# Kernel tuning notes

Measured on AMD Instinct MI355X. Metric: run time of the kernel, lower is better.

Reference implementation:

```python
import jax, jax.numpy as jnp
import numpy as np

N, M, D, H = 16, 1024, 64, 4  # batch, num_node, dim_in==dim_hid, num_head
NEG_SLOPE = 0.2


def setup_inputs() -> dict:
    key = jax.random.key(0)
    ks = jax.random.split(key, 10)
    s = 1.0 / np.sqrt(D)
    inp = {
        "x": jax.random.normal(ks[0], (N, M, D), dtype=jnp.float32),
        "edge": jnp.zeros((N, M, M), dtype=jnp.float32),  # unused by the module
        # stacked per-head Linear(dim_in, dim_hid) params: weight (H, D_out, D_in), bias (H, D_out)
        "Wk": (jax.random.normal(ks[1], (H, D, D), dtype=jnp.float32) * s),
        "bk": (jax.random.normal(ks[2], (H, D), dtype=jnp.float32) * s),
        "Wq": (jax.random.normal(ks[3], (H, D, D), dtype=jnp.float32) * s),
        "bq": (jax.random.normal(ks[4], (H, D), dtype=jnp.float32) * s),
        "Wv": (jax.random.normal(ks[5], (H, D, D), dtype=jnp.float32) * s),
        "bv": (jax.random.normal(ks[6], (H, D), dtype=jnp.float32) * s),
        # decoder: Linear(dim_hid*num_head -> dim_in)
        "Wdec": (jax.random.normal(ks[7], (D, H * D), dtype=jnp.float32) / np.sqrt(H * D)),
        "bdec": (jax.random.normal(ks[8], (D,), dtype=jnp.float32) / np.sqrt(H * D)),
    }
    return inp


def reference(x, edge, Wk, bk, Wq, bq, Wv, bv, Wdec, bdec):
    # x: (N, M, D). Per head h: K = x @ Wk[h].T + bk[h], etc.
    K = jnp.einsum("nmd,hed->nhme", x, Wk) + bk[None, :, None, :]  # (N,H,M,D)
    Q = jnp.einsum("nmd,hed->nhme", x, Wq) + bq[None, :, None, :]
    V = jnp.einsum("nmd,hed->nhme", x, Wv) + bv[None, :, None, :]
    # alpha[n,h,i,j] = K[n,h,i] . Q[n,h,j]  (sender=K row i, receiver=Q row j)
    alpha = jnp.einsum("nhie,nhje->nhij", K, Q)  # (N,H,M,M)
    alpha = jax.nn.leaky_relu(alpha, NEG_SLOPE)
    alpha = jax.nn.softmax(alpha, axis=-1)
    agg = jnp.einsum("nhij,nhje->nhie", alpha, V)  # (N,H,M,D)
    dx = jax.nn.leaky_relu(agg, NEG_SLOPE) - x[:, None, :, :]  # (N,H,M,D)
    # concat heads along feature dim (head 0 first): (N, M, H*D)
    dx = dx.transpose(0, 2, 1, 3).reshape(N, M, H * D)
    return dx @ Wdec.T + bdec  # (N, M, D)
```

## Files before the change

### kernel.cpp

```cpp
#include <hip/hip_runtime.h>
#include <hip/hip_bf16.h>


#define NB 16
#define MM 1024
#define DD 64
#define HH 4
#define NEG 0.2f
#define AST 72
#define DST 264

typedef __attribute__((ext_vector_type(8))) short bf16x8;
typedef __attribute__((ext_vector_type(8))) _Float16 f16x8;
typedef __attribute__((ext_vector_type(16))) float f32x16;

__device__ inline unsigned short f2bf(float f) {
  unsigned int u = __builtin_bit_cast(unsigned int, f);
  unsigned int r = (u + 0x7FFFu + ((u >> 16) & 1u)) >> 16;
  return (unsigned short)r;
}
__device__ inline unsigned short f2h(float f) {
  _Float16 h = (_Float16)f;
  return __builtin_bit_cast(unsigned short, h);
}

__global__ __launch_bounds__(256) void prep_kernel(
    const float* __restrict__ Wk, const float* __restrict__ Wq,
    const float* __restrict__ Wv, const float* __restrict__ Wdec,
    unsigned short* __restrict__ Wf) {
  const int idx = (blockIdx.x * 256 + threadIdx.x) * 4;
  const int seg = idx >> 14, local = idx & 16383;
  const float* src = seg == 0 ? Wk : seg == 1 ? Wq : seg == 2 ? Wv : Wdec;
  float4 v = *(const float4*)&src[local];
  unsigned short p[4] = {f2h(v.x), f2h(v.y), f2h(v.z), f2h(v.w)};
  *(uint2*)&Wf[idx] = *(uint2*)p;
}

__global__ __launch_bounds__(256) void proj_kernel(
    const float* __restrict__ x, const unsigned short* __restrict__ Wf,
    const float* __restrict__ bk, const float* __restrict__ bq, const float* __restrict__ bv,
    unsigned short* __restrict__ Kf, unsigned short* __restrict__ Qf,
    unsigned short* __restrict__ Vtg) {
  __shared__ unsigned short xs[64 * AST];
  __shared__ unsigned short ob[64 * AST];
  const int t = threadIdx.x;
  const int r0 = blockIdx.x * 64;
  const int combo = blockIdx.y, mat = combo >> 2, h = combo & 3;
  const int n = r0 >> 10, ml = r0 & 1023;
  const float* bias = mat == 0 ? bk : (mat == 1 ? bq : bv);

#pragma unroll
  for (int rep = 0; rep < 2; ++rep) {
    int idx = rep * 256 + t, row = idx >> 3, c8 = (idx & 7) * 8;
    float4 a = *(const float4*)&x[(size_t)(r0 + row) * DD + c8];
    float4 b = *(const float4*)&x[(size_t)(r0 + row) * DD + c8 + 4];
    unsigned short p[8] = {f2h(a.x), f2h(a.y), f2h(a.z), f2h(a.w),
                           f2h(b.x), f2h(b.y), f2h(b.z), f2h(b.w)};
    *(uint4*)&xs[row * AST + c8] = *(uint4*)p;
  }
  __syncthreads();

  const int w = t >> 6, lane = t & 63, m31 = lane & 31, hf = lane >> 5;
  const int mi = w >> 1, ne = w & 1;
  const int ecol = h * 64 + ne * 32 + m31;
  const float bb = bias[ecol];

  f32x16 C;
#pragma unroll
  for (int r = 0; r < 16; ++r) C[r] = 0.f;
#pragma unroll
  for (int ks = 0; ks < 4; ++ks) {
    f16x8 xa = *(f16x8*)&xs[(mi * 32 + m31) * AST + ks * 16 + hf * 8];
    f16x8 wb = *(const f16x8*)&Wf[(size_t)mat * 16384 + (size_t)ecol * DD + ks * 16 + hf * 8];
    C = __builtin_amdgcn_mfma_f32_32x32x16_f16(xa, wb, C, 0, 0, 0);
  }

  if (mat < 2) {
#pragma unroll
    for (int r = 0; r < 16; ++r) {
      int rr = (r & 3) + 8 * (r >> 2) + 4 * hf;
      ob[(mi * 32 + rr) * AST + ne * 32 + m31] = f2h(C[r] + bb);
    }
  } else {
#pragma unroll
    for (int r = 0; r < 16; ++r) {
      int rr = (r & 3) + 8 * (r >> 2) + 4 * hf;
      ob[(ne * 32 + m31) * AST + mi * 32 + rr] = f2bf(C[r] + bb);
    }
  }
  __syncthreads();

  if (mat < 2) {
    unsigned short* dst = mat == 0 ? Kf : Qf;
    const size_t obase = (((size_t)n * HH + h) * MM + ml) * DD;
#pragma unroll
    for (int rep = 0; rep < 2; ++rep) {
      int idx = rep * 256 + t, row = idx >> 3, c8 = (idx & 7) * 8;
      *(uint4*)&dst[obase + (size_t)row * DD + c8] = *(uint4*)&ob[row * AST + c8];
    }
  } else {
    const size_t obase = (((size_t)n * HH + h) * DD) * MM + ml;
#pragma unroll
    for (int rep = 0; rep < 2; ++rep) {
      int idx = rep * 256 + t, row = idx >> 3, c8 = (idx & 7) * 8;
      *(uint4*)&Vtg[obase + (size_t)row * MM + c8] = *(uint4*)&ob[row * AST + c8];
    }
  }
}

__global__ __launch_bounds__(256, 4) void attn_kernel(
    const unsigned short* __restrict__ Kf, const unsigned short* __restrict__ Qf,
    const unsigned short* __restrict__ Vtg, const float* __restrict__ x,
    unsigned short* __restrict__ DX) {
  __shared__ unsigned short qh[64 * AST];
  __shared__ unsigned short vt[64 * AST];
  __shared__ unsigned short ps[64 * AST];
  __shared__ float ls[64];

  const int t = threadIdx.x;
  const int w = t >> 6, lane = t & 63;
  const int m31 = lane & 31, hf = lane >> 5;
  const int ti = w >> 1, tw = w & 1;
  const int i0 = blockIdx.x * 64, h = blockIdx.y, n = blockIdx.z;
  const size_t base = (((size_t)n * HH + h) * MM) * DD;
  const size_t baseT = (((size_t)n * HH + h) * DD) * MM;

  f16x8 kfrag[4];
#pragma unroll
  for (int ks = 0; ks < 4; ++ks)
    kfrag[ks] = *(const f16x8*)&Kf[base + (size_t)(i0 + ti * 32 + m31) * DD + ks * 16 + hf * 8];

  f32x16 agg, accl;
#pragma unroll
  for (int r = 0; r < 16; ++r) { agg[r] = 0.f; accl[r] = 0.f; }
  bf16x8 ones;
#pragma unroll
  for (int r = 0; r < 8; ++r) ones[r] = (short)0x3F80;

  for (int jt = 0; jt < 16; ++jt) {
    const int j0 = jt * 64;
    __syncthreads();
#pragma unroll
    for (int rep = 0; rep < 2; ++rep) {
      int idx = rep * 256 + t, row = idx >> 3, c8 = (idx & 7) * 8;
      *(uint4*)&qh[row * AST + c8] = *(const uint4*)&Qf[base + (size_t)(j0 + row) * DD + c8];
      *(uint4*)&vt[row * AST + c8] = *(const uint4*)&Vtg[baseT + (size_t)row * MM + j0 + c8];
    }
    __syncthreads();

    f32x16 C;
#pragma unroll
    for (int r = 0; r < 16; ++r) C[r] = 0.f;
#pragma unroll
    for (int ks = 0; ks < 4; ++ks) {
      f16x8 qf = *(f16x8*)&qh[(tw * 32 + m31) * AST + ks * 16 + hf * 8];
      C = __builtin_amdgcn_mfma_f32_32x32x16_f16(kfrag[ks], qf, C, 0, 0, 0);
    }
#pragma unroll
    for (int r = 0; r < 16; ++r) {
      float s = C[r];
      s = s > 0.f ? s : NEG * s;
      int rr = (r & 3) + 8 * (r >> 2) + 4 * hf;
      ps[(ti * 32 + rr) * AST + tw * 32 + m31] = f2bf(__expf(s));
    }
    __syncthreads();

#pragma unroll
    for (int ks = 0; ks < 4; ++ks) {
      bf16x8 aP = *(bf16x8*)&ps[(ti * 32 + m31) * AST + ks * 16 + hf * 8];
      bf16x8 bV = *(bf16x8*)&vt[(tw * 32 + m31) * AST + ks * 16 + hf * 8];
      agg = __builtin_amdgcn_mfma_f32_32x32x16_bf16(aP, bV, agg, 0, 0, 0);
      if (tw == 0)
        accl = __builtin_amdgcn_mfma_f32_32x32x16_bf16(aP, ones, accl, 0, 0, 0);
    }
  }

  if (tw == 0 && m31 == 0) {
#pragma unroll
    for (int r = 0; r < 16; ++r) {
      int rr = (r & 3) + 8 * (r >> 2) + 4 * hf;
      ls[ti * 32 + rr] = accl[r];
    }
  }
  __syncthreads();

#pragma unroll
  for (int r = 0; r < 16; ++r) {
    int rr = (r & 3) + 8 * (r >> 2) + 4 * hf;
    float l = ls[ti * 32 + rr];
    float v = agg[r] / l;
    v = v > 0.f ? v : NEG * v;
    v -= x[((size_t)n * MM + i0 + ti * 32 + rr) * DD + tw * 32 + m31];
    ps[(ti * 32 + rr) * AST + tw * 32 + m31] = f2h(v);
  }
  __syncthreads();
#pragma unroll
  for (int rep = 0; rep < 2; ++rep) {
    int idx = rep * 256 + t, row = idx >> 3, c8 = (idx & 7) * 8;
    *(uint4*)&DX[((size_t)n * MM + i0 + row) * (HH * DD) + h * DD + c8] =
        *(uint4*)&ps[row * AST + c8];
  }
}

__global__ __launch_bounds__(256) void dec_kernel(
    const unsigned short* __restrict__ DX, const unsigned short* __restrict__ Wdf,
    const float* __restrict__ bdec, float* __restrict__ out) {
  __shared__ unsigned short dxs[64 * DST];
  const int t = threadIdx.x;
  const int w = t >> 6, lane = t & 63, m31 = lane & 31, hf = lane >> 5;
  const int mi = w >> 1, nd = w & 1;
  const int r0 = blockIdx.x * 64;
#pragma unroll
  for (int rep = 0; rep < 8; ++rep) {
    int idx = rep * 256 + t, row = idx >> 5, c8 = (idx & 31) * 8;
    *(uint4*)&dxs[row * DST + c8] = *(const uint4*)&DX[(size_t)(r0 + row) * 256 + c8];
  }
  __syncthreads();
  const float bb = bdec[nd * 32 + m31];
  f32x16 C;
#pragma unroll
  for (int r = 0; r < 16; ++r) C[r] = 0.f;
#pragma unroll
  for (int ks = 0; ks < 16; ++ks) {
    f16x8 aD = *(f16x8*)&dxs[(mi * 32 + m31) * DST + ks * 16 + hf * 8];
    f16x8 bW = *(const f16x8*)&Wdf[(size_t)(nd * 32 + m31) * 256 + ks * 16 + hf * 8];
    C = __builtin_amdgcn_mfma_f32_32x32x16_f16(aD, bW, C, 0, 0, 0);
  }
#pragma unroll
  for (int r = 0; r < 16; ++r) {
    int rr = (r & 3) + 8 * (r >> 2) + 4 * hf;
    out[(size_t)(r0 + mi * 32 + rr) * DD + nd * 32 + m31] = C[r] + bb;
  }
}

extern "C" void kernel_launch(void* const* d_in, const int* in_sizes, int n_in,
                              void* d_out, int out_size, void* d_ws, size_t ws_size,
                              hipStream_t stream) {
  const float* x    = (const float*)d_in[0];
  const float* Wk   = (const float*)d_in[2];
  const float* bk   = (const float*)d_in[3];
  const float* Wq   = (const float*)d_in[4];
  const float* bq   = (const float*)d_in[5];
  const float* Wv   = (const float*)d_in[6];
  const float* bv   = (const float*)d_in[7];
  const float* Wdec = (const float*)d_in[8];
  const float* bdec = (const float*)d_in[9];
  float* out = (float*)d_out;

  const size_t seg = (size_t)NB * HH * MM * DD;
  unsigned short* Kf  = (unsigned short*)d_ws;
  unsigned short* Qf  = Kf + seg;
  unsigned short* Vt  = Qf + seg;
  unsigned short* DXp = Vt + seg;
  unsigned short* Wf  = DXp + seg;
  unsigned short* Wdf = Wf + 3 * 16384;

  prep_kernel<<<64, 256, 0, stream>>>(Wk, Wq, Wv, Wdec, Wf);
  proj_kernel<<<dim3(256, 12), 256, 0, stream>>>(x, Wf, bk, bq, bv, Kf, Qf, Vt);
  attn_kernel<<<dim3(16, HH, NB), 256, 0, stream>>>(Kf, Qf, Vt, x, DXp);
  dec_kernel<<<NB * MM / 64, 256, 0, stream>>>(DXp, Wdf, bdec, out);
}
```

Before: 162.1 us.

## Restructure attention to keep P in registers and drop weight prep kernel

The attention kernel now gives each wave 32 query rows of a 128-row tile. It computes the transposed score tile (Q·K) so the exponentiated probabilities stay in registers, packed to bf16 and exchanged across the half-waves with lane shuffles. This removes the shared-memory P staging, one barrier per tile, and the ones-vector MFMA used for row sums, which are now accumulated with scalar adds. The separate weight-conversion kernel is also removed: proj and dec convert fp32 weights to fp16 inline, saving a launch at the cost of redundant conversions and wider weight loads. The grid for attention is halved, so fewer blocks run, each doing more work.

```diff
diff --git a/kernel.cpp b/kernel.cpp
--- a/kernel.cpp
+++ b/kernel.cpp
@@ -16,28 +16,23 @@
 
 __device__ inline unsigned short f2bf(float f) {
   unsigned int u = __builtin_bit_cast(unsigned int, f);
-  unsigned int r = (u + 0x7FFFu + ((u >> 16) & 1u)) >> 16;
-  return (unsigned short)r;
+  return (unsigned short)((u + 0x7FFFu + ((u >> 16) & 1u)) >> 16);
 }
 __device__ inline unsigned short f2h(float f) {
   _Float16 h = (_Float16)f;
   return __builtin_bit_cast(unsigned short, h);
 }
-
-__global__ __launch_bounds__(256) void prep_kernel(
-    const float* __restrict__ Wk, const float* __restrict__ Wq,
-    const float* __restrict__ Wv, const float* __restrict__ Wdec,
-    unsigned short* __restrict__ Wf) {
-  const int idx = (blockIdx.x * 256 + threadIdx.x) * 4;
-  const int seg = idx >> 14, local = idx & 16383;
-  const float* src = seg == 0 ? Wk : seg == 1 ? Wq : seg == 2 ? Wv : Wdec;
-  float4 v = *(const float4*)&src[local];
-  unsigned short p[4] = {f2h(v.x), f2h(v.y), f2h(v.z), f2h(v.w)};
-  *(uint2*)&Wf[idx] = *(uint2*)p;
+__device__ inline unsigned int pack_bf16(float a, float b) {
+  unsigned int ua = __builtin_bit_cast(unsigned int, a);
+  unsigned int ub = __builtin_bit_cast(unsigned int, b);
+  ua = (ua + 0x7FFFu + ((ua >> 16) & 1u)) >> 16;
+  ub = (ub + 0x7FFFu + ((ub >> 16) & 1u)) & 0xFFFF0000u;
+  return ua | ub;
 }
 
 __global__ __launch_bounds__(256) void proj_kernel(
-    const float* __restrict__ x, const unsigned short* __restrict__ Wf,
+    const float* __restrict__ x,
+    const float* __restrict__ Wk, const float* __restrict__ Wq, const float* __restrict__ Wv,
     const float* __restrict__ bk, const float* __restrict__ bq, const float* __restrict__ bv,
     unsigned short* __restrict__ Kf, unsigned short* __restrict__ Qf,
     unsigned short* __restrict__ Vtg) {
@@ -47,6 +42,7 @@
   const int r0 = blockIdx.x * 64;
   const int combo = blockIdx.y, mat = combo >> 2, h = combo & 3;
   const int n = r0 >> 10, ml = r0 & 1023;
+  const float* W = mat == 0 ? Wk : (mat == 1 ? Wq : Wv);
   const float* bias = mat == 0 ? bk : (mat == 1 ? bq : bv);
 
 #pragma unroll
@@ -71,7 +67,11 @@
 #pragma unroll
   for (int ks = 0; ks < 4; ++ks) {
     f16x8 xa = *(f16x8*)&xs[(mi * 32 + m31) * AST + ks * 16 + hf * 8];
-    f16x8 wb = *(const f16x8*)&Wf[(size_t)mat * 16384 + (size_t)ecol * DD + ks * 16 + hf * 8];
+    float4 wa = *(const float4*)&W[(size_t)ecol * DD + ks * 16 + hf * 8];
+    float4 wc = *(const float4*)&W[(size_t)ecol * DD + ks * 16 + hf * 8 + 4];
+    f16x8 wb;
+    wb[0] = (_Float16)wa.x; wb[1] = (_Float16)wa.y; wb[2] = (_Float16)wa.z; wb[3] = (_Float16)wa.w;
+    wb[4] = (_Float16)wc.x; wb[5] = (_Float16)wc.y; wb[6] = (_Float16)wc.z; wb[7] = (_Float16)wc.w;
     C = __builtin_amdgcn_mfma_f32_32x32x16_f16(xa, wb, C, 0, 0, 0);
   }
 
@@ -108,34 +108,31 @@
   }
 }
 
-__global__ __launch_bounds__(256, 4) void attn_kernel(
+__global__ __launch_bounds__(256) void attn_kernel(
     const unsigned short* __restrict__ Kf, const unsigned short* __restrict__ Qf,
     const unsigned short* __restrict__ Vtg, const float* __restrict__ x,
     unsigned short* __restrict__ DX) {
-  __shared__ unsigned short qh[64 * AST];
-  __shared__ unsigned short vt[64 * AST];
-  __shared__ unsigned short ps[64 * AST];
-  __shared__ float ls[64];
+  __shared__ unsigned short smem[2 * 64 * AST];
+  __shared__ float ls[128];
+  unsigned short* qh = smem;
+  unsigned short* vt = smem + 64 * AST;
 
   const int t = threadIdx.x;
-  const int w = t >> 6, lane = t & 63;
-  const int m31 = lane & 31, hf = lane >> 5;
-  const int ti = w >> 1, tw = w & 1;
-  const int i0 = blockIdx.x * 64, h = blockIdx.y, n = blockIdx.z;
+  const int w = t >> 6, lane = t & 63, m31 = lane & 31, hf = lane >> 5;
+  const int i0 = blockIdx.x * 128, h = blockIdx.y, n = blockIdx.z;
   const size_t base = (((size_t)n * HH + h) * MM) * DD;
   const size_t baseT = (((size_t)n * HH + h) * DD) * MM;
-
-  f16x8 kfrag[4];
+  const int iw = i0 + w * 32 + m31;
+
+  f16x8 kf[4];
 #pragma unroll
   for (int ks = 0; ks < 4; ++ks)
-    kfrag[ks] = *(const f16x8*)&Kf[base + (size_t)(i0 + ti * 32 + m31) * DD + ks * 16 + hf * 8];
-
-  f32x16 agg, accl;
-#pragma unroll
-  for (int r = 0; r < 16; ++r) { agg[r] = 0.f; accl[r] = 0.f; }
-  bf16x8 ones;
-#pragma unroll
-  for (int r = 0; r < 8; ++r) ones[r] = (short)0x3F80;
+    kf[ks] = *(const f16x8*)&Kf[base + (size_t)iw * DD + ks * 16 + hf * 8];
+
+  f32x16 agg0, agg1;
+#pragma unroll
+  for (int r = 0; r < 16; ++r) { agg0[r] = 0.f; agg1[r] = 0.f; }
+  float lsum = 0.f;
 
   for (int jt = 0; jt < 16; ++jt) {
     const int j0 = jt * 64;
@@ -148,62 +145,83 @@
     }
     __syncthreads();
 
-    f32x16 C;
-#pragma unroll
-    for (int r = 0; r < 16; ++r) C[r] = 0.f;
+    unsigned int pk[16];
+#pragma unroll
+    for (int t2 = 0; t2 < 2; ++t2) {
+      f32x16 C;
+#pragma unroll
+      for (int r = 0; r < 16; ++r) C[r] = 0.f;
+#pragma unroll
+      for (int ks = 0; ks < 4; ++ks) {
+        f16x8 qa = *(f16x8*)&qh[(t2 * 32 + m31) * AST + ks * 16 + hf * 8];
+        C = __builtin_amdgcn_mfma_f32_32x32x16_f16(qa, kf[ks], C, 0, 0, 0);
+      }
+#pragma unroll
+      for (int g = 0; g < 4; ++g) {
+        float p0 = C[4 * g + 0], p1 = C[4 * g + 1], p2 = C[4 * g + 2], p3 = C[4 * g + 3];
+        p0 = __expf(fmaxf(p0, NEG * p0));
+        p1 = __expf(fmaxf(p1, NEG * p1));
+        p2 = __expf(fmaxf(p2, NEG * p2));
+        p3 = __expf(fmaxf(p3, NEG * p3));
+        lsum += (p0 + p1) + (p2 + p3);
+        pk[t2 * 8 + g * 2]     = pack_bf16(p0, p1);
+        pk[t2 * 8 + g * 2 + 1] = pack_bf16(p2, p3);
+      }
+    }
+
 #pragma unroll
     for (int ks = 0; ks < 4; ++ks) {
-      f16x8 qf = *(f16x8*)&qh[(tw * 32 + m31) * AST + ks * 16 + hf * 8];
-      C = __builtin_amdgcn_mfma_f32_32x32x16_f16(kfrag[ks], qf, C, 0, 0, 0);
-    }
-#pragma unroll
-    for (int r = 0; r < 16; ++r) {
-      float s = C[r];
-      s = s > 0.f ? s : NEG * s;
-      int rr = (r & 3) + 8 * (r >> 2) + 4 * hf;
-      ps[(ti * 32 + rr) * AST + tw * 32 + m31] = f2bf(__expf(s));
-    }
-    __syncthreads();
-
-#pragma unroll
-    for (int ks = 0; ks < 4; ++ks) {
-      bf16x8 aP = *(bf16x8*)&ps[(ti * 32 + m31) * AST + ks * 16 + hf * 8];
-      bf16x8 bV = *(bf16x8*)&vt[(tw * 32 + m31) * AST + ks * 16 + hf * 8];
-      agg = __builtin_amdgcn_mfma_f32_32x32x16_bf16(aP, bV, agg, 0, 0, 0);
-      if (tw == 0)
-        accl = __builtin_amdgcn_mfma_f32_32x32x16_bf16(aP, ones, accl, 0, 0, 0);
-    }
-  }
-
-  if (tw == 0 && m31 == 0) {
+      const int b = (ks >> 1) * 8, gl2 = (ks & 1) * 4, gh2 = gl2 + 2;
+      unsigned int sA = hf ? pk[b + gl2]     : pk[b + gh2];
+      unsigned int sB = hf ? pk[b + gl2 + 1] : pk[b + gh2 + 1];
+      unsigned int rA = (unsigned int)__shfl_xor((int)sA, 32);
+      unsigned int rB = (unsigned int)__shfl_xor((int)sB, 32);
+      union { unsigned int u[4]; bf16x8 v; } cv;
+      cv.u[0] = hf ? rA : pk[b + gl2];
+      cv.u[1] = hf ? rB : pk[b + gl2 + 1];
+      cv.u[2] = hf ? pk[b + gh2]     : rA;
+      cv.u[3] = hf ? pk[b + gh2 + 1] : rB;
+      bf16x8 bV0 = *(bf16x8*)&vt[m31 * AST + ks * 16 + hf * 8];
+      bf16x8 bV1 = *(bf16x8*)&vt[(32 + m31) * AST + ks * 16 + hf * 8];
+      agg0 = __builtin_amdgcn_mfma_f32_32x32x16_bf16(cv.v, bV0, agg0, 0, 0, 0);
+      agg1 = __builtin_amdgcn_mfma_f32_32x32x16_bf16(cv.v, bV1, agg1, 0, 0, 0);
+    }
+  }
+
+  lsum += __shfl_xor(lsum, 32);
+  if (hf == 0) ls[w * 32 + m31] = lsum;
+  __syncthreads();
+
+  unsigned short* dxb = smem;
+  float invl[16];
+#pragma unroll
+  for (int r = 0; r < 16; ++r) {
+    int rr = (r & 3) + 8 * (r >> 2) + 4 * hf;
+    invl[r] = 1.0f / ls[w * 32 + rr];
+  }
+#pragma unroll
+  for (int half = 0; half < 2; ++half) {
+    const int e = half * 32 + m31;
 #pragma unroll
     for (int r = 0; r < 16; ++r) {
       int rr = (r & 3) + 8 * (r >> 2) + 4 * hf;
-      ls[ti * 32 + rr] = accl[r];
-    }
-  }
-  __syncthreads();
-
-#pragma unroll
-  for (int r = 0; r < 16; ++r) {
-    int rr = (r & 3) + 8 * (r >> 2) + 4 * hf;
-    float l = ls[ti * 32 + rr];
-    float v = agg[r] / l;
-    v = v > 0.f ? v : NEG * v;
-    v -= x[((size_t)n * MM + i0 + ti * 32 + rr) * DD + tw * 32 + m31];
-    ps[(ti * 32 + rr) * AST + tw * 32 + m31] = f2h(v);
-  }
-  __syncthreads();
-#pragma unroll
-  for (int rep = 0; rep < 2; ++rep) {
+      float v = (half ? agg1[r] : agg0[r]) * invl[r];
+      v = fmaxf(v, NEG * v);
+      v -= x[((size_t)n * MM + i0 + w * 32 + rr) * DD + e];
+      dxb[(w * 32 + rr) * AST + e] = f2h(v);
+    }
+  }
+  __syncthreads();
+#pragma unroll
+  for (int rep = 0; rep < 4; ++rep) {
     int idx = rep * 256 + t, row = idx >> 3, c8 = (idx & 7) * 8;
     *(uint4*)&DX[((size_t)n * MM + i0 + row) * (HH * DD) + h * DD + c8] =
-        *(uint4*)&ps[row * AST + c8];
+        *(uint4*)&dxb[row * AST + c8];
   }
 }
 
 __global__ __launch_bounds__(256) void dec_kernel(
-    const unsigned short* __restrict__ DX, const unsigned short* __restrict__ Wdf,
+    const unsigned short* __restrict__ DX, const float* __restrict__ Wdec,
     const float* __restrict__ bdec, float* __restrict__ out) {
   __shared__ unsigned short dxs[64 * DST];
   const int t = threadIdx.x;
@@ -223,7 +241,11 @@
 #pragma unroll
   for (int ks = 0; ks < 16; ++ks) {
     f16x8 aD = *(f16x8*)&dxs[(mi * 32 + m31) * DST + ks * 16 + hf * 8];
-    f16x8 bW = *(const f16x8*)&Wdf[(size_t)(nd * 32 + m31) * 256 + ks * 16 + hf * 8];
+    float4 wa = *(const float4*)&Wdec[(size_t)(nd * 32 + m31) * 256 + ks * 16 + hf * 8];
+    float4 wc = *(const float4*)&Wdec[(size_t)(nd * 32 + m31) * 256 + ks * 16 + hf * 8 + 4];
+    f16x8 bW;
+    bW[0] = (_Float16)wa.x; bW[1] = (_Float16)wa.y; bW[2] = (_Float16)wa.z; bW[3] = (_Float16)wa.w;
+    bW[4] = (_Float16)wc.x; bW[5] = (_Float16)wc.y; bW[6] = (_Float16)wc.z; bW[7] = (_Float16)wc.w;
     C = __builtin_amdgcn_mfma_f32_32x32x16_f16(aD, bW, C, 0, 0, 0);
   }
 #pragma unroll
@@ -252,11 +274,8 @@
   unsigned short* Qf  = Kf + seg;
   unsigned short* Vt  = Qf + seg;
   unsigned short* DXp = Vt + seg;
-  unsigned short* Wf  = DXp + seg;
-  unsigned short* Wdf = Wf + 3 * 16384;
-
-  prep_kernel<<<64, 256, 0, stream>>>(Wk, Wq, Wv, Wdec, Wf);
-  proj_kernel<<<dim3(256, 12), 256, 0, stream>>>(x, Wf, bk, bq, bv, Kf, Qf, Vt);
-  attn_kernel<<<dim3(16, HH, NB), 256, 0, stream>>>(Kf, Qf, Vt, x, DXp);
-  dec_kernel<<<NB * MM / 64, 256, 0, stream>>>(DXp, Wdf, bdec, out);
-}
+
+  proj_kernel<<<dim3(256, 12), 256, 0, stream>>>(x, Wk, Wq, Wv, bk, bq, bv, Kf, Qf, Vt);
+  attn_kernel<<<dim3(8, HH, NB), 256, 0, stream>>>(Kf, Qf, Vt, x, DXp);
+  dec_kernel<<<NB * MM / 64, 256, 0, stream>>>(DXp, Wdec, bdec, out);
+}
```

Result: slower. 193.3 us (+19.3%).
